# Optimization experiments

Hardware: AMD Instinct MI355X
Metric: run time of the kernel (lower is better)

## Reference

```python
import jax, jax.numpy as jnp
import numpy as np
from jax import lax

N = 4194304  # batch of FP16 values, each encoded as 16 spike bits

# MSB-first bit weights / shift amounts for the [S,E4..E0,M9..M0] layout
_POW = np.array([1 << (15 - i) for i in range(16)], dtype=np.int32)
_SHIFTS = np.array([15 - i for i in range(16)], dtype=np.int32)


def _pack(bits):
    """[..., 16] {0,1} float bits (MSB first) -> float16 scalar per row."""
    b = jnp.round(bits).astype(jnp.int32)
    u = jnp.sum(b * _POW, axis=-1).astype(jnp.uint16)
    return lax.bitcast_convert_type(u, jnp.float16)


def _unpack(f):
    """float16 [...] -> [..., 16] {0,1} float32 bits (MSB first)."""
    u = lax.bitcast_convert_type(f, jnp.uint16).astype(jnp.int32)
    return ((u[..., None] >> _SHIFTS) & 1).astype(jnp.float32)


def _sample_bits(key, n):
    bits = jax.random.bernoulli(key, 0.5, (n, 16)).astype(jnp.float32)
    # avoid exponent == 31 (Inf/NaN encodings) so outputs are well-defined finite fp16
    all_ones = jnp.prod(bits[:, 1:6], axis=-1, keepdims=True)
    return bits.at[:, 5:6].set(bits[:, 5:6] * (1.0 - all_ones))


def setup_inputs() -> dict:
    key = jax.random.key(0)
    ka, kb = jax.random.split(key)
    return {"A": _sample_bits(ka, N), "B": _sample_bits(kb, N)}


def reference(A, B):
    # The SNN gate network implements an IEEE-754 FP16 adder (round-to-nearest-even,
    # subnormal support, overflow/underflow handling) over bit-encoded operands.
    # fp16 add computed via fp32 is bit-exact here (24 >= 2*11+2, Figueroa's theorem),
    # which is what XLA does for float16 on CPU.
    s = _pack(A) + _pack(B)
    return _unpack(s)
```

## Files before the change

kernel.cpp:

```cpp
#include <hip/hip_runtime.h>
#include <hip/hip_fp16.h>


typedef float float4_n __attribute__((ext_vector_type(4)));

__global__ __launch_bounds__(256) void spike_fp16_add_kernel(
    const float4* __restrict__ A, const float4* __restrict__ B,
    float4* __restrict__ O, int nf4)
{
    const int lane = threadIdx.x & 63;
    const int waveBase = ((blockIdx.x * blockDim.x + threadIdx.x) >> 6) * 256;
    const int q = lane & 3;
    const int sh = 12 - 4 * q;
    const int idx = waveBase + lane;

    if (waveBase + 255 < nf4) {
        float4 a[4], b[4];
        #pragma unroll
        for (int k = 0; k < 4; ++k) a[k] = A[idx + k * 64];
        #pragma unroll
        for (int k = 0; k < 4; ++k) b[k] = B[idx + k * 64];

        #pragma unroll
        for (int k = 0; k < 4; ++k) {
            uint32_t ua = (((uint32_t)a[k].x << 3) | ((uint32_t)a[k].y << 2) |
                           ((uint32_t)a[k].z << 1) |  (uint32_t)a[k].w) << sh;
            uint32_t ub = (((uint32_t)b[k].x << 3) | ((uint32_t)b[k].y << 2) |
                           ((uint32_t)b[k].z << 1) |  (uint32_t)b[k].w) << sh;

            ua |= (uint32_t)__shfl_xor((int)ua, 1);
            ua |= (uint32_t)__shfl_xor((int)ua, 2);
            ub |= (uint32_t)__shfl_xor((int)ub, 1);
            ub |= (uint32_t)__shfl_xor((int)ub, 2);

            float fa = __half2float(__ushort_as_half((unsigned short)ua));
            float fb = __half2float(__ushort_as_half((unsigned short)ub));
            uint32_t us = (uint32_t)__half_as_ushort(__float2half_rn(fa + fb));

            uint32_t ns = (us >> sh) & 0xFu;
            float4_n o;
            o.x = (float)((ns >> 3) & 1u);
            o.y = (float)((ns >> 2) & 1u);
            o.z = (float)((ns >> 1) & 1u);
            o.w = (float)( ns       & 1u);
            __builtin_nontemporal_store(o, (float4_n*)&O[idx + k * 64]);
        }
    } else {
        for (int k = 0; k < 4; ++k) {
            int f4 = idx + k * 64;
            uint32_t ua = 0, ub = 0;
            if (f4 < nf4) {
                float4 a = A[f4], b = B[f4];
                ua = (((uint32_t)a.x << 3) | ((uint32_t)a.y << 2) |
                      ((uint32_t)a.z << 1) |  (uint32_t)a.w) << sh;
                ub = (((uint32_t)b.x << 3) | ((uint32_t)b.y << 2) |
                      ((uint32_t)b.z << 1) |  (uint32_t)b.w) << sh;
            }
            ua |= (uint32_t)__shfl_xor((int)ua, 1);
            ua |= (uint32_t)__shfl_xor((int)ua, 2);
            ub |= (uint32_t)__shfl_xor((int)ub, 1);
            ub |= (uint32_t)__shfl_xor((int)ub, 2);
            float fa = __half2float(__ushort_as_half((unsigned short)ua));
            float fb = __half2float(__ushort_as_half((unsigned short)ub));
            uint32_t us = (uint32_t)__half_as_ushort(__float2half_rn(fa + fb));
            uint32_t ns = (us >> sh) & 0xFu;
            float4 o;
            o.x = (float)((ns >> 3) & 1u);
            o.y = (float)((ns >> 2) & 1u);
            o.z = (float)((ns >> 1) & 1u);
            o.w = (float)( ns       & 1u);
            if (f4 < nf4) O[f4] = o;
        }
    }
}

extern "C" void kernel_launch(void* const* d_in, const int* in_sizes, int n_in,
                              void* d_out, int out_size, void* d_ws, size_t ws_size,
                              hipStream_t stream) {
    const float4* A = (const float4*)d_in[0];
    const float4* B = (const float4*)d_in[1];
    float4* O = (float4*)d_out;

    int nf4 = in_sizes[0] / 4;
    int block = 256;
    int threads = (nf4 + 3) / 4;
    int grid = (threads + block - 1) / block;
    spike_fp16_add_kernel<<<grid, block, 0, stream>>>(A, B, O, nf4);
}
```

Baseline: 583.1 us.

## Use persistent grid-stride waves with double-buffered prefetch and integer bit extraction

Replaces the one-tile-per-wave launch with a fixed grid of 1536 blocks whose waves stride across the data. Each wave prefetches the next 256-float4 tile of A and B while it processes the current one. Inputs are read as uint4 and bits are taken from the float exponent with shifts instead of float-to-int conversions. Output stores switch from nontemporal to normal stores, and the extra prefetch registers may lower occupancy.

```diff
diff --git a/kernel.cpp b/kernel.cpp
--- a/kernel.cpp
+++ b/kernel.cpp
@@ -2,59 +2,82 @@
 #include <hip/hip_fp16.h>
 
 
-typedef float float4_n __attribute__((ext_vector_type(4)));
-
 __global__ __launch_bounds__(256) void spike_fp16_add_kernel(
-    const float4* __restrict__ A, const float4* __restrict__ B,
-    float4* __restrict__ O, int nf4)
+    const uint4* __restrict__ A, const uint4* __restrict__ B,
+    float4* __restrict__ O, int nf4, int waveStride)
 {
     const int lane = threadIdx.x & 63;
-    const int waveBase = ((blockIdx.x * blockDim.x + threadIdx.x) >> 6) * 256;
+    const int waveId = (blockIdx.x * blockDim.x + threadIdx.x) >> 6;
     const int q = lane & 3;
     const int sh = 12 - 4 * q;
-    const int idx = waveBase + lane;
+    const int nf4_full = nf4 & ~255;
 
-    if (waveBase + 255 < nf4) {
-        float4 a[4], b[4];
+    int base = waveId * 256;
+
+    if (base < nf4_full) {
+        uint4 a0[4], b0[4], a1[4], b1[4];
+        int idx = base + lane;
         #pragma unroll
-        for (int k = 0; k < 4; ++k) a[k] = A[idx + k * 64];
+        for (int k = 0; k < 4; ++k) a0[k] = A[idx + k * 64];
         #pragma unroll
-        for (int k = 0; k < 4; ++k) b[k] = B[idx + k * 64];
+        for (int k = 0; k < 4; ++k) b0[k] = B[idx + k * 64];
 
-        #pragma unroll
-        for (int k = 0; k < 4; ++k) {
-            uint32_t ua = (((uint32_t)a[k].x << 3) | ((uint32_t)a[k].y << 2) |
-                           ((uint32_t)a[k].z << 1) |  (uint32_t)a[k].w) << sh;
-            uint32_t ub = (((uint32_t)b[k].x << 3) | ((uint32_t)b[k].y << 2) |
-                           ((uint32_t)b[k].z << 1) |  (uint32_t)b[k].w) << sh;
+        while (true) {
+            const int nbase = base + waveStride;
+            const bool hasNext = (nbase < nf4_full);
+            const int nidx = idx + waveStride;
+            if (hasNext) {
+                #pragma unroll
+                for (int k = 0; k < 4; ++k) a1[k] = A[nidx + k * 64];
+                #pragma unroll
+                for (int k = 0; k < 4; ++k) b1[k] = B[nidx + k * 64];
+            }
 
-            ua |= (uint32_t)__shfl_xor((int)ua, 1);
-            ua |= (uint32_t)__shfl_xor((int)ua, 2);
-            ub |= (uint32_t)__shfl_xor((int)ub, 1);
-            ub |= (uint32_t)__shfl_xor((int)ub, 2);
+            #pragma unroll
+            for (int k = 0; k < 4; ++k) {
+                uint32_t ua = (((a0[k].x >> 20) & 8u) | ((a0[k].y >> 21) & 4u) |
+                               ((a0[k].z >> 22) & 2u) | ((a0[k].w >> 23) & 1u)) << sh;
+                uint32_t ub = (((b0[k].x >> 20) & 8u) | ((b0[k].y >> 21) & 4u) |
+                               ((b0[k].z >> 22) & 2u) | ((b0[k].w >> 23) & 1u)) << sh;
 
-            float fa = __half2float(__ushort_as_half((unsigned short)ua));
-            float fb = __half2float(__ushort_as_half((unsigned short)ub));
-            uint32_t us = (uint32_t)__half_as_ushort(__float2half_rn(fa + fb));
+                ua |= (uint32_t)__shfl_xor((int)ua, 1);
+                ua |= (uint32_t)__shfl_xor((int)ua, 2);
+                ub |= (uint32_t)__shfl_xor((int)ub, 1);
+                ub |= (uint32_t)__shfl_xor((int)ub, 2);
 
-            uint32_t ns = (us >> sh) & 0xFu;
-            float4_n o;
-            o.x = (float)((ns >> 3) & 1u);
-            o.y = (float)((ns >> 2) & 1u);
-            o.z = (float)((ns >> 1) & 1u);
-            o.w = (float)( ns       & 1u);
-            __builtin_nontemporal_store(o, (float4_n*)&O[idx + k * 64]);
+                float fa = __half2float(__ushort_as_half((unsigned short)ua));
+                float fb = __half2float(__ushort_as_half((unsigned short)ub));
+                uint32_t us = (uint32_t)__half_as_ushort(__float2half_rn(fa + fb));
+
+                uint32_t ns = (us >> sh) & 0xFu;
+                float4 o;
+                o.x = (float)((ns >> 3) & 1u);
+                o.y = (float)((ns >> 2) & 1u);
+                o.z = (float)((ns >> 1) & 1u);
+                o.w = (float)( ns       & 1u);
+                O[idx + k * 64] = o;
+            }
+
+            if (!hasNext) break;
+            #pragma unroll
+            for (int k = 0; k < 4; ++k) { a0[k] = a1[k]; b0[k] = b1[k]; }
+            base = nbase;
+            idx = nidx;
         }
-    } else {
-        for (int k = 0; k < 4; ++k) {
-            int f4 = idx + k * 64;
+    }
+
+    const int tail = nf4 - nf4_full;
+    if (tail > 0) {
+        const int gid = blockIdx.x * blockDim.x + threadIdx.x;
+        if (gid < 256) {
+            const int f4 = nf4_full + gid;
             uint32_t ua = 0, ub = 0;
             if (f4 < nf4) {
-                float4 a = A[f4], b = B[f4];
-                ua = (((uint32_t)a.x << 3) | ((uint32_t)a.y << 2) |
-                      ((uint32_t)a.z << 1) |  (uint32_t)a.w) << sh;
-                ub = (((uint32_t)b.x << 3) | ((uint32_t)b.y << 2) |
-                      ((uint32_t)b.z << 1) |  (uint32_t)b.w) << sh;
+                uint4 a = A[f4], b = B[f4];
+                ua = (((a.x >> 20) & 8u) | ((a.y >> 21) & 4u) |
+                      ((a.z >> 22) & 2u) | ((a.w >> 23) & 1u)) << sh;
+                ub = (((b.x >> 20) & 8u) | ((b.y >> 21) & 4u) |
+                      ((b.z >> 22) & 2u) | ((b.w >> 23) & 1u)) << sh;
             }
             ua |= (uint32_t)__shfl_xor((int)ua, 1);
             ua |= (uint32_t)__shfl_xor((int)ua, 2);
@@ -77,13 +100,15 @@
 extern "C" void kernel_launch(void* const* d_in, const int* in_sizes, int n_in,
                               void* d_out, int out_size, void* d_ws, size_t ws_size,
                               hipStream_t stream) {
-    const float4* A = (const float4*)d_in[0];
-    const float4* B = (const float4*)d_in[1];
+    const uint4* A = (const uint4*)d_in[0];
+    const uint4* B = (const uint4*)d_in[1];
     float4* O = (float4*)d_out;
 
     int nf4 = in_sizes[0] / 4;
     int block = 256;
-    int threads = (nf4 + 3) / 4;
-    int grid = (threads + block - 1) / block;
-    spike_fp16_add_kernel<<<grid, block, 0, stream>>>(A, B, O, nf4);
+    int grid = 1536;
+    int totalWaves = grid * (block / 64);
+    int waveStride = totalWaves * 256;
+
+    spike_fp16_add_kernel<<<grid, block, 0, stream>>>(A, B, O, nf4, waveStride);
 }
```

Result: no change. 583.5 us (+0.1%).

## Split into sum kernel writing fp16 workspace and separate expand kernel

Applied to the files above, without the earlier changes.

Replaces the fused shuffle-based kernel with two kernels when enough workspace exists. The first kernel has each thread read a full 64-byte row of A and B, extract the bits by testing the float exponent bit, and write a 16-bit sum into the workspace. The second kernel reads the sums back and expands them into float4 output bits. This removes cross-lane shuffles but adds a second launch and a workspace round trip, drops the nontemporal stores, and makes the per-thread loads in the first kernel strided rather than coalesced.

```diff
diff --git a/kernel.cpp b/kernel.cpp
--- a/kernel.cpp
+++ b/kernel.cpp
@@ -2,88 +2,132 @@
 #include <hip/hip_fp16.h>
 
 
-typedef float float4_n __attribute__((ext_vector_type(4)));
+__global__ __launch_bounds__(256) void spike_p1_sum_kernel(
+    const uint4* __restrict__ A, const uint4* __restrict__ B,
+    unsigned short* __restrict__ S, int nrows)
+{
+    int r = blockIdx.x * blockDim.x + threadIdx.x;
+    if (r >= nrows) return;
+    const size_t base = (size_t)r * 4;
 
-__global__ __launch_bounds__(256) void spike_fp16_add_kernel(
-    const float4* __restrict__ A, const float4* __restrict__ B,
-    float4* __restrict__ O, int nf4)
+    uint4 a0 = A[base + 0], a1 = A[base + 1], a2 = A[base + 2], a3 = A[base + 3];
+    uint4 b0 = B[base + 0], b1 = B[base + 1], b2 = B[base + 2], b3 = B[base + 3];
+
+    uint32_t ua =
+        (((a0.x >> 23) & 1u) << 15) | (((a0.y >> 23) & 1u) << 14) |
+        (((a0.z >> 23) & 1u) << 13) | (((a0.w >> 23) & 1u) << 12) |
+        (((a1.x >> 23) & 1u) << 11) | (((a1.y >> 23) & 1u) << 10) |
+        (((a1.z >> 23) & 1u) <<  9) | (((a1.w >> 23) & 1u) <<  8) |
+        (((a2.x >> 23) & 1u) <<  7) | (((a2.y >> 23) & 1u) <<  6) |
+        (((a2.z >> 23) & 1u) <<  5) | (((a2.w >> 23) & 1u) <<  4) |
+        (((a3.x >> 23) & 1u) <<  3) | (((a3.y >> 23) & 1u) <<  2) |
+        (((a3.z >> 23) & 1u) <<  1) |  ((a3.w >> 23) & 1u);
+    uint32_t ub =
+        (((b0.x >> 23) & 1u) << 15) | (((b0.y >> 23) & 1u) << 14) |
+        (((b0.z >> 23) & 1u) << 13) | (((b0.w >> 23) & 1u) << 12) |
+        (((b1.x >> 23) & 1u) << 11) | (((b1.y >> 23) & 1u) << 10) |
+        (((b1.z >> 23) & 1u) <<  9) | (((b1.w >> 23) & 1u) <<  8) |
+        (((b2.x >> 23) & 1u) <<  7) | (((b2.y >> 23) & 1u) <<  6) |
+        (((b2.z >> 23) & 1u) <<  5) | (((b2.w >> 23) & 1u) <<  4) |
+        (((b3.x >> 23) & 1u) <<  3) | (((b3.y >> 23) & 1u) <<  2) |
+        (((b3.z >> 23) & 1u) <<  1) |  ((b3.w >> 23) & 1u);
+
+    float fa = __half2float(__ushort_as_half((unsigned short)ua));
+    float fb = __half2float(__ushort_as_half((unsigned short)ub));
+    S[r] = __half_as_ushort(__float2half_rn(fa + fb));
+}
+
+__global__ __launch_bounds__(256) void spike_p2_expand_kernel(
+    const unsigned short* __restrict__ S, float4* __restrict__ O, int nf4)
 {
     const int lane = threadIdx.x & 63;
     const int waveBase = ((blockIdx.x * blockDim.x + threadIdx.x) >> 6) * 256;
-    const int q = lane & 3;
-    const int sh = 12 - 4 * q;
+    const int sh = 12 - 4 * (lane & 3);
     const int idx = waveBase + lane;
 
     if (waveBase + 255 < nf4) {
-        float4 a[4], b[4];
+        uint32_t us[4];
         #pragma unroll
-        for (int k = 0; k < 4; ++k) a[k] = A[idx + k * 64];
-        #pragma unroll
-        for (int k = 0; k < 4; ++k) b[k] = B[idx + k * 64];
-
+        for (int k = 0; k < 4; ++k) us[k] = S[(idx + k * 64) >> 2];
         #pragma unroll
         for (int k = 0; k < 4; ++k) {
-            uint32_t ua = (((uint32_t)a[k].x << 3) | ((uint32_t)a[k].y << 2) |
-                           ((uint32_t)a[k].z << 1) |  (uint32_t)a[k].w) << sh;
-            uint32_t ub = (((uint32_t)b[k].x << 3) | ((uint32_t)b[k].y << 2) |
-                           ((uint32_t)b[k].z << 1) |  (uint32_t)b[k].w) << sh;
-
-            ua |= (uint32_t)__shfl_xor((int)ua, 1);
-            ua |= (uint32_t)__shfl_xor((int)ua, 2);
-            ub |= (uint32_t)__shfl_xor((int)ub, 1);
-            ub |= (uint32_t)__shfl_xor((int)ub, 2);
-
-            float fa = __half2float(__ushort_as_half((unsigned short)ua));
-            float fb = __half2float(__ushort_as_half((unsigned short)ub));
-            uint32_t us = (uint32_t)__half_as_ushort(__float2half_rn(fa + fb));
-
-            uint32_t ns = (us >> sh) & 0xFu;
-            float4_n o;
-            o.x = (float)((ns >> 3) & 1u);
-            o.y = (float)((ns >> 2) & 1u);
-            o.z = (float)((ns >> 1) & 1u);
-            o.w = (float)( ns       & 1u);
-            __builtin_nontemporal_store(o, (float4_n*)&O[idx + k * 64]);
-        }
-    } else {
-        for (int k = 0; k < 4; ++k) {
-            int f4 = idx + k * 64;
-            uint32_t ua = 0, ub = 0;
-            if (f4 < nf4) {
-                float4 a = A[f4], b = B[f4];
-                ua = (((uint32_t)a.x << 3) | ((uint32_t)a.y << 2) |
-                      ((uint32_t)a.z << 1) |  (uint32_t)a.w) << sh;
-                ub = (((uint32_t)b.x << 3) | ((uint32_t)b.y << 2) |
-                      ((uint32_t)b.z << 1) |  (uint32_t)b.w) << sh;
-            }
-            ua |= (uint32_t)__shfl_xor((int)ua, 1);
-            ua |= (uint32_t)__shfl_xor((int)ua, 2);
-            ub |= (uint32_t)__shfl_xor((int)ub, 1);
-            ub |= (uint32_t)__shfl_xor((int)ub, 2);
-            float fa = __half2float(__ushort_as_half((unsigned short)ua));
-            float fb = __half2float(__ushort_as_half((unsigned short)ub));
-            uint32_t us = (uint32_t)__half_as_ushort(__float2half_rn(fa + fb));
-            uint32_t ns = (us >> sh) & 0xFu;
+            uint32_t ns = (us[k] >> sh) & 0xFu;
             float4 o;
             o.x = (float)((ns >> 3) & 1u);
             o.y = (float)((ns >> 2) & 1u);
             o.z = (float)((ns >> 1) & 1u);
             o.w = (float)( ns       & 1u);
-            if (f4 < nf4) O[f4] = o;
+            O[idx + k * 64] = o;
         }
+    } else {
+        for (int k = 0; k < 4; ++k) {
+            int f4 = idx + k * 64;
+            if (f4 < nf4) {
+                uint32_t ns = ((uint32_t)S[f4 >> 2] >> sh) & 0xFu;
+                float4 o;
+                o.x = (float)((ns >> 3) & 1u);
+                o.y = (float)((ns >> 2) & 1u);
+                o.z = (float)((ns >> 1) & 1u);
+                o.w = (float)( ns       & 1u);
+                O[f4] = o;
+            }
+        }
+    }
+}
+
+__global__ __launch_bounds__(256) void spike_fused_kernel(
+    const uint4* __restrict__ A, const uint4* __restrict__ B,
+    float4* __restrict__ O, int nf4)
+{
+    const int lane = threadIdx.x & 63;
+    const int waveBase = ((blockIdx.x * blockDim.x + threadIdx.x) >> 6) * 256;
+    const int sh = 12 - 4 * (lane & 3);
+    const int idx = waveBase + lane;
+
+    for (int k = 0; k < 4; ++k) {
+        int f4 = idx + k * 64;
+        uint32_t ua = 0, ub = 0;
+        if (f4 < nf4) {
+            uint4 a = A[f4], b = B[f4];
+            ua = (((a.x >> 20) & 8u) | ((a.y >> 21) & 4u) |
+                  ((a.z >> 22) & 2u) | ((a.w >> 23) & 1u)) << sh;
+            ub = (((b.x >> 20) & 8u) | ((b.y >> 21) & 4u) |
+                  ((b.z >> 22) & 2u) | ((b.w >> 23) & 1u)) << sh;
+        }
+        ua |= (uint32_t)__shfl_xor((int)ua, 1);
+        ua |= (uint32_t)__shfl_xor((int)ua, 2);
+        ub |= (uint32_t)__shfl_xor((int)ub, 1);
+        ub |= (uint32_t)__shfl_xor((int)ub, 2);
+        float fa = __half2float(__ushort_as_half((unsigned short)ua));
+        float fb = __half2float(__ushort_as_half((unsigned short)ub));
+        uint32_t us = (uint32_t)__half_as_ushort(__float2half_rn(fa + fb));
+        uint32_t ns = (us >> sh) & 0xFu;
+        float4 o;
+        o.x = (float)((ns >> 3) & 1u);
+        o.y = (float)((ns >> 2) & 1u);
+        o.z = (float)((ns >> 1) & 1u);
+        o.w = (float)( ns       & 1u);
+        if (f4 < nf4) O[f4] = o;
     }
 }
 
 extern "C" void kernel_launch(void* const* d_in, const int* in_sizes, int n_in,
                               void* d_out, int out_size, void* d_ws, size_t ws_size,
                               hipStream_t stream) {
-    const float4* A = (const float4*)d_in[0];
-    const float4* B = (const float4*)d_in[1];
-    float4* O = (float4*)d_out;
+    int nrows = in_sizes[0] / 16;
+    int nf4 = nrows * 4;
+    int block = 256;
 
-    int nf4 = in_sizes[0] / 4;
-    int block = 256;
-    int threads = (nf4 + 3) / 4;
-    int grid = (threads + block - 1) / block;
-    spike_fp16_add_kernel<<<grid, block, 0, stream>>>(A, B, O, nf4);
+    if (ws_size >= (size_t)nrows * sizeof(unsigned short)) {
+        unsigned short* S = (unsigned short*)d_ws;
+        int grid1 = (nrows + block - 1) / block;
+        spike_p1_sum_kernel<<<grid1, block, 0, stream>>>(
+            (const uint4*)d_in[0], (const uint4*)d_in[1], S, nrows);
+        int grid2 = ((nf4 + 3) / 4 + block - 1) / block;
+        spike_p2_expand_kernel<<<grid2, block, 0, stream>>>(S, (float4*)d_out, nf4);
+    } else {
+        int grid = ((nf4 + 3) / 4 + block - 1) / block;
+        spike_fused_kernel<<<grid, block, 0, stream>>>(
+            (const uint4*)d_in[0], (const uint4*)d_in[1], (float4*)d_out, nf4);
+    }
 }
```

Measured after the change: 598.4 us. 2.6% more time.
